# Kernel tuning notes

Hardware: AMD Instinct MI355X
Metric: run time of the kernel (lower is better)

## Reference

```python
import jax, jax.numpy as jnp
import numpy as np

D_MODEL = 1024
N_HEADS = 16
FFN_DIM = 4096
EPS = 1e-5


def layer_norm(x, g, b):
    m = jnp.mean(x, axis=-1, keepdims=True)
    v = jnp.mean((x - m) ** 2, axis=-1, keepdims=True)
    return (x - m) * jax.lax.rsqrt(v + EPS) * g + b


def setup_inputs() -> dict:
    key = jax.random.key(0)
    ks = jax.random.split(key, 8)
    B, S, D, F = 4, 1024, D_MODEL, FFN_DIM
    return {
        "k": jax.random.normal(ks[0], (B, S, D), jnp.float32),
        "v": jax.random.normal(ks[1], (B, S, D), jnp.float32),
        "q": jax.random.normal(ks[2], (B, S, D), jnp.float32),
        "r": jax.random.normal(ks[3], (B, S, D), jnp.float32),
        "Wf": jax.random.normal(ks[4], (D, D), jnp.float32) * 0.02,
        "bf": jnp.zeros((D,), jnp.float32),
        "g1": jnp.ones((D,), jnp.float32),
        "b1": jnp.zeros((D,), jnp.float32),
        "W1": jax.random.normal(ks[5], (D, F), jnp.float32) * 0.02,
        "bw1": jnp.zeros((F,), jnp.float32),
        "W2": jax.random.normal(ks[6], (F, D), jnp.float32) * 0.02,
        "bw2": jnp.zeros((D,), jnp.float32),
        "g2": jnp.ones((D,), jnp.float32),
        "b2": jnp.zeros((D,), jnp.float32),
    }


def reference(k, v, q, r, Wf, bf, g1, b1, W1, bw1, W2, bw2, g2, b2):
    B, S, D = k.shape
    H = N_HEADS
    d = D // H
    # Encoder layer calls attention(k, q, v, r) against signature (k, v, q, r):
    # inner_q = outer v, inner_v = outer q  (faithful to the source quirk).
    kk = k.reshape(B * H, -1, d)   # raw view-based head split, as in torch
    vv = q.reshape(B * H, -1, d)
    qq = v.reshape(B * H, -1, d)
    scale = d ** 0.5  # NOTE: source MULTIPLIES by sqrt(d)
    scores = jnp.einsum('bqd,bkd->bqk', qq, kk) * scale  # [B*H, S, S]
    attn = jax.nn.softmax(scores, axis=-1)
    ctx = jnp.einsum('bqk,bkd->bqd', attn, vv).reshape(B, -1, D)
    out = ctx @ Wf + bf
    x = layer_norm(r + out, g1, b1)
    # FFN: 1x1 Conv1d pair == dense matmuls
    h = jax.nn.relu(x @ W1 + bw1)
    y = h @ W2 + bw2
    output = layer_norm(x + y, g2, b2)
    return (output, attn)
```

## Files before the change

kernel.cpp:

```cpp
#include <hip/hip_runtime.h>
#include <hip/hip_bf16.h>
#include <cstdint>

typedef __attribute__((ext_vector_type(8))) __bf16 bf16x8;
typedef __attribute__((ext_vector_type(4))) __bf16 bf16x4;
typedef __attribute__((ext_vector_type(4))) float f32x4;
typedef unsigned int uint32;
typedef unsigned short uint16;

#define LDS_AS __attribute__((address_space(3)))
#define GLB_AS __attribute__((address_space(1)))

static __device__ __forceinline__ void gld_lds16(const void* g, LDS_AS char* l) {
  __builtin_amdgcn_global_load_lds((const GLB_AS uint32*)g, (LDS_AS uint32*)l, 16, 0, 0);
}

#define MFMA(a, b, c) __builtin_amdgcn_mfma_f32_16x16x32_bf16((a), (b), (c), 0, 0, 0)

static __device__ __forceinline__ f32x4 mfma3(bf16x8 ah, bf16x8 al, bf16x8 bh,
                                              bf16x8 bl, f32x4 c) {
  c = MFMA(ah, bh, c);
  c = MFMA(al, bh, c);
  c = MFMA(ah, bl, c);
  return c;
}

static __device__ __forceinline__ uint32 pack_bf16(float a, float b) {
  __bf16 ha = (__bf16)a, hb = (__bf16)b;
  return (uint32)__builtin_bit_cast(uint16, ha) |
         ((uint32)__builtin_bit_cast(uint16, hb) << 16);
}

#define KB(row, colbyte) ((((row) * 128 + (colbyte))) ^ (((row) & 7) << 4))

__global__ __launch_bounds__(256) void prep_all(
    const float* __restrict__ K, const float* __restrict__ V,
    char* __restrict__ KH, char* __restrict__ KL, char* __restrict__ VT,
    const float* __restrict__ Wf, __bf16* __restrict__ WFT,
    const float* __restrict__ W1, __bf16* __restrict__ W1T,
    const float* __restrict__ W2, __bf16* __restrict__ W2T) {
  int b = blockIdx.x;
  if (b < 1024) {
    int kt = b & 15, h = b >> 4;
    const float* src = K + (size_t)h * 65536 + kt * 4096;
    char* dh = KH + (size_t)(h * 16 + kt) * 8192;
    char* dl = KL + (size_t)(h * 16 + kt) * 8192;
    int r = threadIdx.x >> 2, cq = threadIdx.x & 3;
    const float* sp = src + r * 64 + cq * 16;
    bf16x8 h0, l0, h1, l1;
#pragma unroll
    for (int j = 0; j < 8; ++j) {
      float x0 = sp[j], x1 = sp[8 + j];
      __bf16 a = (__bf16)x0, bb = (__bf16)x1;
      h0[j] = a; l0[j] = (__bf16)(x0 - (float)a);
      h1[j] = bb; l1[j] = (__bf16)(x1 - (float)bb);
    }
    int sw = (r & 7) << 4;
    int o0 = (r * 128 + cq * 32) ^ sw;
    int o1 = (r * 128 + cq * 32 + 16) ^ sw;
    *(bf16x8*)(dh + o0) = h0;
    *(bf16x8*)(dh + o1) = h1;
    *(bf16x8*)(dl + o0) = l0;
    *(bf16x8*)(dl + o1) = l1;
    return;
  }
  if (b < 2048) {
    b -= 1024;
    int kt = b & 15, h = b >> 4;
    const float* src = V + (size_t)h * 65536 + kt * 4096;
    char* dv = VT + (size_t)(h * 16 + kt) * 8192;
    int kp = threadIdx.x >> 3, dq = threadIdx.x & 7;
    const float* s0 = src + (2 * kp) * 64 + dq * 8;
    const float* s1 = s0 + 64;
#pragma unroll
    for (int j = 0; j < 8; ++j) {
      uint32 pk = pack_bf16(s0[j], s1[j]);
      int d = dq * 8 + j;
      *(uint32*)(dv + ((d * 128 + kp * 4) ^ ((d & 7) << 4))) = pk;
    }
    return;
  }
  const float* in;
  __bf16* out;
  int R, C, bx, by;
  if (b < 3072) {
    b -= 2048; in = Wf; out = WFT; R = 1024; C = 1024;
    bx = (b & 31) * 32; by = (b >> 5) * 32;
  } else if (b < 7168) {
    b -= 3072; in = W1; out = W1T; R = 1024; C = 4096;
    bx = (b & 127) * 32; by = (b >> 7) * 32;
  } else {
    b -= 7168; in = W2; out = W2T; R = 4096; C = 1024;
    bx = (b & 31) * 32; by = (b >> 5) * 32;
  }
  __shared__ float tile[32][33];
  int tx = threadIdx.x & 31, ty = threadIdx.x >> 5;
  for (int i = ty; i < 32; i += 8)
    tile[i][tx] = in[(size_t)(by + i) * C + bx + tx];
  __syncthreads();
  for (int i = ty; i < 32; i += 8)
    out[(size_t)(bx + i) * R + by + tx] = (__bf16)tile[tx][i];
}

__global__ __launch_bounds__(512, 4) void attn_v8(
    const float* __restrict__ Qin, const char* __restrict__ KHimg,
    const char* __restrict__ KLimg, const char* __restrict__ VTimg,
    float* __restrict__ attn_out, __bf16* __restrict__ ctx_out)
{
  __shared__ __attribute__((aligned(16))) char KsH[2][8192];
  __shared__ __attribute__((aligned(16))) char KsL[2][8192];
  __shared__ __attribute__((aligned(16))) char Vt[2][8192];
  __shared__ __attribute__((aligned(16))) __bf16 PsH[8][16][72];

  const int tid = threadIdx.x;
  const int l = tid & 63, w = tid >> 6;
  const int lr = l & 15, q4 = l >> 4;
  const int swz = (blockIdx.x & 7) * 64 + (blockIdx.x >> 3);
  const int g = swz >> 3, rb = swz & 7;
  const size_t base = (size_t)g * 65536;
  const char* khb = KHimg + (size_t)g * 131072;
  const char* klb = KLimg + (size_t)g * 131072;
  const char* vtb = VTimg + (size_t)g * 131072;

  const float* qp = Qin + base + (size_t)(rb * 128 + w * 16 + lr) * 64;
  f32x4 qv[4];
#pragma unroll
  for (int j = 0; j < 2; ++j) {
    qv[j] = *(const f32x4*)&qp[q4 * 8 + j * 4];
    qv[2 + j] = *(const f32x4*)&qp[32 + q4 * 8 + j * 4];
  }

  gld_lds16(khb + 0 * 8192 + tid * 16, (LDS_AS char*)&KsH[0][0] + tid * 16);
  gld_lds16(klb + 0 * 8192 + tid * 16, (LDS_AS char*)&KsL[0][0] + tid * 16);

  bf16x8 aqh0, aql0, aqh1, aql1;
#pragma unroll
  for (int j = 0; j < 8; ++j) {
    float x0 = qv[j >> 2][j & 3];
    float x1 = qv[2 + (j >> 2)][j & 3];
    __bf16 h0 = (__bf16)x0, h1 = (__bf16)x1;
    aqh0[j] = h0; aql0[j] = (__bf16)(x0 - (float)h0);
    aqh1[j] = h1; aql1[j] = (__bf16)(x1 - (float)h1);
  }

  float m_r[4], ll_r[4];
#pragma unroll
  for (int r = 0; r < 4; ++r) { m_r[r] = -1e30f; ll_r[r] = 0.f; }

  for (int kt = 0; kt < 16; ++kt) {
    const int buf = kt & 1;
    if (kt < 15) {
      gld_lds16(khb + (kt + 1) * 8192 + tid * 16,
                (LDS_AS char*)&KsH[buf ^ 1][0] + tid * 16);
      gld_lds16(klb + (kt + 1) * 8192 + tid * 16,
                (LDS_AS char*)&KsL[buf ^ 1][0] + tid * 16);
      asm volatile("s_waitcnt vmcnt(2)" ::: "memory");
    } else {
      asm volatile("s_waitcnt vmcnt(0)" ::: "memory");
    }
    __builtin_amdgcn_s_barrier();
    const char* ksh = KsH[buf];
    const char* ksl = KsL[buf];
    f32x4 c[4];
#pragma unroll
    for (int nf = 0; nf < 4; ++nf) {
      int row = nf * 16 + lr;
      f32x4 cc = {0.f, 0.f, 0.f, 0.f};
      cc = mfma3(aqh0, aql0, *(const bf16x8*)(ksh + KB(row, q4 * 16)),
                 *(const bf16x8*)(ksl + KB(row, q4 * 16)), cc);
      cc = mfma3(aqh1, aql1, *(const bf16x8*)(ksh + KB(row, 64 + q4 * 16)),
                 *(const bf16x8*)(ksl + KB(row, 64 + q4 * 16)), cc);
      c[nf] = cc;
    }
#pragma unroll
    for (int r = 0; r < 4; ++r) {
      float s0 = c[0][r] * 8.f, s1 = c[1][r] * 8.f;
      float s2 = c[2][r] * 8.f, s3 = c[3][r] * 8.f;
      float lm = fmaxf(fmaxf(s0, s1), fmaxf(s2, s3));
      float mnew = fmaxf(m_r[r], lm);
      ll_r[r] = ll_r[r] * __expf(m_r[r] - mnew) +
                (__expf(s0 - mnew) + __expf(s1 - mnew) +
                 __expf(s2 - mnew) + __expf(s3 - mnew));
      m_r[r] = mnew;
    }
    __builtin_amdgcn_s_barrier();
  }
  float inv_l[4];
#pragma unroll
  for (int r = 0; r < 4; ++r) {
    float M = m_r[r];
#pragma unroll
    for (int o = 1; o < 16; o <<= 1) M = fmaxf(M, __shfl_xor(M, o, 64));
    float ls = ll_r[r] * __expf(m_r[r] - M);
#pragma unroll
    for (int o = 1; o < 16; o <<= 1) ls += __shfl_xor(ls, o, 64);
    m_r[r] = M;
    inv_l[r] = 1.f / ls;
  }

  f32x4 co[4];
#pragma unroll
  for (int cf = 0; cf < 4; ++cf) co[cf] = (f32x4){0.f, 0.f, 0.f, 0.f};

  gld_lds16(khb + 0 * 8192 + tid * 16, (LDS_AS char*)&KsH[0][0] + tid * 16);
  gld_lds16(klb + 0 * 8192 + tid * 16, (LDS_AS char*)&KsL[0][0] + tid * 16);
  gld_lds16(vtb + 0 * 8192 + tid * 16, (LDS_AS char*)&Vt[0][0] + tid * 16);

  for (int kt = 0; kt < 16; ++kt) {
    const int buf = kt & 1;
    if (kt < 15) {
      gld_lds16(khb + (kt + 1) * 8192 + tid * 16,
                (LDS_AS char*)&KsH[buf ^ 1][0] + tid * 16);
      gld_lds16(klb + (kt + 1) * 8192 + tid * 16,
                (LDS_AS char*)&KsL[buf ^ 1][0] + tid * 16);
      gld_lds16(vtb + (kt + 1) * 8192 + tid * 16,
                (LDS_AS char*)&Vt[buf ^ 1][0] + tid * 16);
    }
    if (kt == 0) {
      asm volatile("s_waitcnt vmcnt(3)" ::: "memory");
    } else if (kt < 15) {
      asm volatile("s_waitcnt vmcnt(19)" ::: "memory");
    } else {
      asm volatile("s_waitcnt vmcnt(16)" ::: "memory");
    }
    __builtin_amdgcn_s_barrier();
    const char* ksh = KsH[buf];
    const char* ksl = KsL[buf];
    const char* vts = Vt[buf];
#pragma unroll
    for (int nf = 0; nf < 4; ++nf) {
      int row = nf * 16 + lr;
      f32x4 cc = {0.f, 0.f, 0.f, 0.f};
      cc = mfma3(aqh0, aql0, *(const bf16x8*)(ksh + KB(row, q4 * 16)),
                 *(const bf16x8*)(ksl + KB(row, q4 * 16)), cc);
      cc = mfma3(aqh1, aql1, *(const bf16x8*)(ksh + KB(row, 64 + q4 * 16)),
                 *(const bf16x8*)(ksl + KB(row, 64 + q4 * 16)), cc);
#pragma unroll
      for (int r = 0; r < 4; ++r) {
        float p = __expf(cc[r] * 8.f - m_r[r]) * inv_l[r];
        PsH[w][q4 * 4 + r][nf * 16 + lr] = (__bf16)p;
        int arow = rb * 128 + w * 16 + q4 * 4 + r;
        __builtin_nontemporal_store(
            p, &attn_out[((size_t)(g * 1024 + arow)) * 1024 + kt * 64 + nf * 16 + lr]);
      }
    }
#pragma unroll
    for (int kk = 0; kk < 2; ++kk) {
      bf16x8 ph = *(const bf16x8*)&PsH[w][lr][kk * 32 + q4 * 8];
#pragma unroll
      for (int cf = 0; cf < 4; ++cf) {
        bf16x8 vt = *(const bf16x8*)(vts + KB(cf * 16 + lr, kk * 64 + q4 * 16));
        co[cf] = MFMA(ph, vt, co[cf]);
      }
    }
    __builtin_amdgcn_s_barrier();
  }
#pragma unroll
  for (int cf = 0; cf < 4; ++cf)
#pragma unroll
    for (int r = 0; r < 4; ++r) {
      int i = rb * 128 + w * 16 + q4 * 4 + r;
      ctx_out[((size_t)(g * 1024 + i)) * 64 + cf * 16 + lr] = (__bf16)co[cf][r];
    }
}

template <int EPI, int BM>
__global__ __launch_bounds__(256) void gemm_db(
    const __bf16* __restrict__ A, const __bf16* __restrict__ Bt,
    const float* __restrict__ bias, const float* __restrict__ Res,
    __bf16* __restrict__ Outb,
    int M, int N, int K, int Kloop, int nbx, int tiles_per_out)
{
  constexpr int MF = BM / 32;
  constexpr int ELEMS = BM * 64 + 8192;
  __shared__ __attribute__((aligned(16))) __bf16 sm[2][ELEMS];
  const int tid = threadIdx.x;
  const int l = tid & 63, w = tid >> 6;
  const int lr = l & 15, lkb = (l >> 4) * 8;
  const int nwg = gridDim.x;
  const int swz = (blockIdx.x & 7) * (nwg >> 3) + (blockIdx.x >> 3);
  const int ks = swz / tiles_per_out;
  const int tile = swz % tiles_per_out;
  const int m0 = (tile / nbx) * BM, n0 = (tile % nbx) * 128;
  const int kbase = ks * Kloop;
  const int wr = (w >> 1) * (BM / 2), wc = (w & 1) * 64;

  f32x4 acc[MF][4];
  f32x4 zero = {0.f, 0.f, 0.f, 0.f};
#pragma unroll
  for (int m = 0; m < MF; ++m)
#pragma unroll
    for (int n = 0; n < 4; ++n) acc[m][n] = zero;

  const int nkt = Kloop >> 6;

#define GSTAGE(BUF, KT)                                                        \
  {                                                                            \
    LDS_AS char* dst = (LDS_AS char*)&sm[(BUF)][0];                            \
    _Pragma("unroll") for (int it = 0; it < MF; ++it) {                        \
      int slot = it * 256 + tid;                                               \
      int row = slot >> 3, cb = slot & 7;                                      \
      gld_lds16(&A[(size_t)(m0 + row) * K + kbase + (KT) * 64 + cb * 8],       \
                dst + slot * 16);                                              \
    }                                                                          \
    _Pragma("unroll") for (int it = 0; it < 4; ++it) {                         \
      int slot = it * 256 + tid;                                               \
      int row = slot >> 3, cb = slot & 7;                                      \
      gld_lds16(&Bt[(size_t)(n0 + row) * K + kbase + (KT) * 64 + cb * 8],      \
                dst + BM * 128 + slot * 16);                                   \
    }                                                                          \
  }

  GSTAGE(0, 0);
  for (int kt = 0; kt < nkt; ++kt) {
    const int buf = kt & 1;
    if (kt < nkt - 1) {
      GSTAGE(buf ^ 1, kt + 1);
      if (BM == 64) {
        asm volatile("s_waitcnt vmcnt(6)" ::: "memory");
      } else {
        asm volatile("s_waitcnt vmcnt(8)" ::: "memory");
      }
    } else {
      asm volatile("s_waitcnt vmcnt(0)" ::: "memory");
    }
    __builtin_amdgcn_s_barrier();
    const __bf16* s = &sm[buf][0];
#pragma unroll
    for (int kk = 0; kk < 2; ++kk) {
      bf16x8 a[MF], b[4];
#pragma unroll
      for (int m = 0; m < MF; ++m)
        a[m] = *(const bf16x8*)&s[(wr + m * 16 + lr) * 64 + kk * 32 + lkb];
#pragma unroll
      for (int n = 0; n < 4; ++n)
        b[n] = *(const bf16x8*)&s[BM * 64 + (wc + n * 16 + lr) * 64 + kk * 32 + lkb];
#pragma unroll
      for (int m = 0; m < MF; ++m)
#pragma unroll
        for (int n = 0; n < 4; ++n) acc[m][n] = MFMA(a[m], b[n], acc[m][n]);
    }
    __builtin_amdgcn_s_barrier();
  }
#undef GSTAGE

  __bf16* outp = (EPI == 5) ? Outb + (size_t)ks * M * N : Outb;
#pragma unroll
  for (int n = 0; n < 4; ++n) {
    int gcol = n0 + wc + n * 16 + lr;
    float bc = (EPI == 5) ? 0.f : bias[gcol];
#pragma unroll
    for (int m = 0; m < MF; ++m) {
      int grow = m0 + wr + m * 16 + (l >> 4) * 4;
#pragma unroll
      for (int r = 0; r < 4; ++r) {
        float v = acc[m][n][r] + bc;
        size_t o = (size_t)(grow + r) * N + gcol;
        if (EPI == 1) {
          outp[o] = (__bf16)fmaxf(v, 0.f);
        } else if (EPI == 4) {
          outp[o] = (__bf16)(v + Res[o]);
        } else {
          outp[o] = (__bf16)v;
        }
      }
    }
  }
}

__global__ __launch_bounds__(256) void ln_b2b(
    const __bf16* __restrict__ in, const float* __restrict__ gam,
    const float* __restrict__ bet, __bf16* __restrict__ outB)
{
  __shared__ float red[8];
  const int row = blockIdx.x, t = threadIdx.x;
  bf16x4 vb = ((const bf16x4*)(in + (size_t)row * 1024))[t];
  float v[4];
  float s = 0.f, ss = 0.f;
#pragma unroll
  for (int j = 0; j < 4; ++j) {
    v[j] = (float)vb[j];
    s += v[j];
    ss += v[j] * v[j];
  }
#pragma unroll
  for (int o = 1; o < 64; o <<= 1) {
    s += __shfl_xor(s, o, 64);
    ss += __shfl_xor(ss, o, 64);
  }
  int w = t >> 6, l = t & 63;
  if (l == 0) { red[w] = s; red[4 + w] = ss; }
  __syncthreads();
  float S = red[0] + red[1] + red[2] + red[3];
  float SS = red[4] + red[5] + red[6] + red[7];
  float mean = S * (1.f / 1024.f);
  float var = SS * (1.f / 1024.f) - mean * mean;
  float rstd = rsqrtf(var + 1e-5f);
  bf16x4 ob;
#pragma unroll
  for (int j = 0; j < 4; ++j) {
    int col = t * 4 + j;
    ob[j] = (__bf16)((v[j] - mean) * rstd * gam[col] + bet[col]);
  }
  ((bf16x4*)(outB + (size_t)row * 1024))[t] = ob;
}

__global__ __launch_bounds__(256) void ln_fuse2(
    const __bf16* __restrict__ P0, const __bf16* __restrict__ P1,
    const float* __restrict__ bias, const __bf16* __restrict__ resB,
    const float* __restrict__ gam, const float* __restrict__ bet,
    float* __restrict__ out)
{
  __shared__ float red[8];
  const int row = blockIdx.x, t = threadIdx.x;
  const size_t ro = (size_t)row * 1024;
  bf16x4 p0 = ((const bf16x4*)(P0 + ro))[t];
  bf16x4 p1 = ((const bf16x4*)(P1 + ro))[t];
  f32x4 bi = ((const f32x4*)bias)[t];
  bf16x4 rb = ((const bf16x4*)(resB + ro))[t];
  f32x4 v;
  float s = 0.f, ss = 0.f;
#pragma unroll
  for (int j = 0; j < 4; ++j) {
    v[j] = (float)p0[j] + (float)p1[j] + bi[j] + (float)rb[j];
    s += v[j];
    ss += v[j] * v[j];
  }
#pragma unroll
  for (int o = 1; o < 64; o <<= 1) {
    s += __shfl_xor(s, o, 64);
    ss += __shfl_xor(ss, o, 64);
  }
  int w = t >> 6, l = t & 63;
  if (l == 0) { red[w] = s; red[4 + w] = ss; }
  __syncthreads();
  float S = red[0] + red[1] + red[2] + red[3];
  float SS = red[4] + red[5] + red[6] + red[7];
  float mean = S * (1.f / 1024.f);
  float var = SS * (1.f / 1024.f) - mean * mean;
  float rstd = rsqrtf(var + 1e-5f);
  f32x4 ov;
#pragma unroll
  for (int j = 0; j < 4; ++j) {
    int col = t * 4 + j;
    ov[j] = (v[j] - mean) * rstd * gam[col] + bet[col];
  }
  ((f32x4*)(out + ro))[t] = ov;
}

extern "C" void kernel_launch(void* const* d_in, const int* in_sizes, int n_in,
                              void* d_out, int out_size, void* d_ws, size_t ws_size,
                              hipStream_t stream) {
  const float* k_in = (const float*)d_in[0];
  const float* v_in = (const float*)d_in[1];
  const float* q_in = (const float*)d_in[2];
  const float* r_in = (const float*)d_in[3];
  const float* Wf = (const float*)d_in[4];
  const float* bf = (const float*)d_in[5];
  const float* g1 = (const float*)d_in[6];
  const float* b1 = (const float*)d_in[7];
  const float* W1 = (const float*)d_in[8];
  const float* bw1 = (const float*)d_in[9];
  const float* W2 = (const float*)d_in[10];
  const float* bw2 = (const float*)d_in[11];
  const float* g2 = (const float*)d_in[12];
  const float* b2 = (const float*)d_in[13];

  float* out0 = (float*)d_out;
  float* attn = out0 + 4194304;

  char* W = (char*)d_ws;
  const size_t MB = 1024 * 1024;
  char* KHimg = W + 0;
  char* KLimg = W + 8 * MB;
  char* VTimg = W + 16 * MB;
  __bf16* WFT = (__bf16*)(W + 24 * MB);
  __bf16* W1T = (__bf16*)(W + 26 * MB);
  __bf16* W2T = (__bf16*)(W + 34 * MB);
  __bf16* CTX = (__bf16*)(W + 42 * MB);
  __bf16* Xb = (__bf16*)(W + 50 * MB);
  __bf16* Hb = (__bf16*)(W + 58 * MB);
  __bf16* T1b = (__bf16*)(W + 90 * MB);
  __bf16* P0b = (__bf16*)(W + 98 * MB);
  __bf16* P1b = (__bf16*)(W + 106 * MB);

  prep_all<<<11264, 256, 0, stream>>>(k_in, q_in, KHimg, KLimg, VTimg,
                                      Wf, WFT, W1, W1T, W2, W2T);

  attn_v8<<<512, 512, 0, stream>>>(v_in, KHimg, KLimg, VTimg, attn, CTX);

  gemm_db<4, 64><<<512, 256, 0, stream>>>(CTX, WFT, bf, r_in, T1b,
                                          4096, 1024, 1024, 1024, 8, 512);
  ln_b2b<<<4096, 256, 0, stream>>>(T1b, g1, b1, Xb);
  gemm_db<1, 128><<<1024, 256, 0, stream>>>(Xb, W1T, bw1, nullptr, Hb,
                                            4096, 4096, 1024, 1024, 32, 1024);
  gemm_db<5, 128><<<512, 256, 0, stream>>>(Hb, W2T, nullptr, nullptr, P0b,
                                           4096, 1024, 4096, 2048, 8, 256);
  ln_fuse2<<<4096, 256, 0, stream>>>(P0b, P1b, bw2, Xb, g2, b2, out0);
}
```

Before: 268.9 us.

## Vectorize attention-prob stores via LDS and split W2 GEMM into four K-slices

```diff
diff --git a/kernel.cpp b/kernel.cpp
--- a/kernel.cpp
+++ b/kernel.cpp
@@ -102,7 +102,7 @@
     out[(size_t)(bx + i) * R + by + tx] = (__bf16)tile[tx][i];
 }
 
-__global__ __launch_bounds__(512, 4) void attn_v8(
+__global__ __launch_bounds__(512, 4) void attn_v9(
     const float* __restrict__ Qin, const char* __restrict__ KHimg,
     const char* __restrict__ KLimg, const char* __restrict__ VTimg,
     float* __restrict__ attn_out, __bf16* __restrict__ ctx_out)
@@ -219,9 +219,9 @@
     if (kt == 0) {
       asm volatile("s_waitcnt vmcnt(3)" ::: "memory");
     } else if (kt < 15) {
-      asm volatile("s_waitcnt vmcnt(19)" ::: "memory");
+      asm volatile("s_waitcnt vmcnt(7)" ::: "memory");
     } else {
-      asm volatile("s_waitcnt vmcnt(16)" ::: "memory");
+      asm volatile("s_waitcnt vmcnt(4)" ::: "memory");
     }
     __builtin_amdgcn_s_barrier();
     const char* ksh = KsH[buf];
@@ -239,9 +239,20 @@
       for (int r = 0; r < 4; ++r) {
         float p = __expf(cc[r] * 8.f - m_r[r]) * inv_l[r];
         PsH[w][q4 * 4 + r][nf * 16 + lr] = (__bf16)p;
-        int arow = rb * 128 + w * 16 + q4 * 4 + r;
+      }
+    }
+    {
+      const int rbase = g * 1024 + rb * 128 + w * 16;
+#pragma unroll
+      for (int it = 0; it < 4; ++it) {
+        int prow = it * 4 + q4;
+        int pcol = lr * 4;
+        bf16x4 pb = *(const bf16x4*)&PsH[w][prow][pcol];
+        f32x4 pf;
+#pragma unroll
+        for (int j = 0; j < 4; ++j) pf[j] = (float)pb[j];
         __builtin_nontemporal_store(
-            p, &attn_out[((size_t)(g * 1024 + arow)) * 1024 + kt * 64 + nf * 16 + lr]);
+            pf, (f32x4*)&attn_out[((size_t)(rbase + prow)) * 1024 + kt * 64 + pcol]);
       }
     }
 #pragma unroll
@@ -405,24 +416,26 @@
   ((bf16x4*)(outB + (size_t)row * 1024))[t] = ob;
 }
 
-__global__ __launch_bounds__(256) void ln_fuse2(
-    const __bf16* __restrict__ P0, const __bf16* __restrict__ P1,
-    const float* __restrict__ bias, const __bf16* __restrict__ resB,
-    const float* __restrict__ gam, const float* __restrict__ bet,
-    float* __restrict__ out)
+__global__ __launch_bounds__(256) void ln_fuse4(
+    const __bf16* __restrict__ Pb, const float* __restrict__ bias,
+    const __bf16* __restrict__ resB, const float* __restrict__ gam,
+    const float* __restrict__ bet, float* __restrict__ out)
 {
   __shared__ float red[8];
   const int row = blockIdx.x, t = threadIdx.x;
   const size_t ro = (size_t)row * 1024;
-  bf16x4 p0 = ((const bf16x4*)(P0 + ro))[t];
-  bf16x4 p1 = ((const bf16x4*)(P1 + ro))[t];
+  bf16x4 p0 = ((const bf16x4*)(Pb + ro))[t];
+  bf16x4 p1 = ((const bf16x4*)(Pb + 4194304 + ro))[t];
+  bf16x4 p2 = ((const bf16x4*)(Pb + 8388608 + ro))[t];
+  bf16x4 p3 = ((const bf16x4*)(Pb + 12582912 + ro))[t];
   f32x4 bi = ((const f32x4*)bias)[t];
   bf16x4 rb = ((const bf16x4*)(resB + ro))[t];
   f32x4 v;
   float s = 0.f, ss = 0.f;
 #pragma unroll
   for (int j = 0; j < 4; ++j) {
-    v[j] = (float)p0[j] + (float)p1[j] + bi[j] + (float)rb[j];
+    v[j] = (float)p0[j] + (float)p1[j] + (float)p2[j] + (float)p3[j] +
+           bi[j] + (float)rb[j];
     s += v[j];
     ss += v[j] * v[j];
   }
@@ -481,20 +494,19 @@
   __bf16* Xb = (__bf16*)(W + 50 * MB);
   __bf16* Hb = (__bf16*)(W + 58 * MB);
   __bf16* T1b = (__bf16*)(W + 90 * MB);
-  __bf16* P0b = (__bf16*)(W + 98 * MB);
-  __bf16* P1b = (__bf16*)(W + 106 * MB);
+  __bf16* Pb = (__bf16*)(W + 98 * MB);
 
   prep_all<<<11264, 256, 0, stream>>>(k_in, q_in, KHimg, KLimg, VTimg,
                                       Wf, WFT, W1, W1T, W2, W2T);
 
-  attn_v8<<<512, 512, 0, stream>>>(v_in, KHimg, KLimg, VTimg, attn, CTX);
+  attn_v9<<<512, 512, 0, stream>>>(v_in, KHimg, KLimg, VTimg, attn, CTX);
 
   gemm_db<4, 64><<<512, 256, 0, stream>>>(CTX, WFT, bf, r_in, T1b,
                                           4096, 1024, 1024, 1024, 8, 512);
   ln_b2b<<<4096, 256, 0, stream>>>(T1b, g1, b1, Xb);
   gemm_db<1, 128><<<1024, 256, 0, stream>>>(Xb, W1T, bw1, nullptr, Hb,
                                             4096, 4096, 1024, 1024, 32, 1024);
-  gemm_db<5, 128><<<512, 256, 0, stream>>>(Hb, W2T, nullptr, nullptr, P0b,
-                                           4096, 1024, 4096, 2048, 8, 256);
-  ln_fuse2<<<4096, 256, 0, stream>>>(P0b, P1b, bw2, Xb, g2, b2, out0);
-}
+  gemm_db<5, 128><<<1024, 256, 0, stream>>>(Hb, W2T, nullptr, nullptr, Pb,
+                                            4096, 1024, 4096, 1024, 8, 256);
+  ln_fuse4<<<4096, 256, 0, stream>>>(Pb, bw2, Xb, g2, b2, out0);
+}
```

Result: faster. 233.8 us (-13.0%).
